# Performance work log

Measured on AMD Instinct MI355X. Metric: run time of the kernel, lower is better.

Reference implementation:

```python
import jax, jax.numpy as jnp
import numpy as np
import math

W = 256
H = 256
N = 1000
C = 1  # grayscale
ALPHA_MAX = 0.999


def _logit(p):
    return jnp.log(p) - jnp.log1p(-p)


def setup_inputs() -> dict:
    key = jax.random.key(0)
    k0, k1, k2, k3, k4 = jax.random.split(key, 5)
    means = jax.random.uniform(k0, (N, 2), dtype=jnp.float32) * W
    scales = jax.random.uniform(k1, (N, 2), dtype=jnp.float32) * 10.0 + 1.0
    quats = jax.random.uniform(k2, (N,), dtype=jnp.float32) * (2.0 * math.pi)  # rotation angle
    rgbs = _logit(jax.random.uniform(k3, (N, C), dtype=jnp.float32) * 0.3 + 0.1)
    opacities = _logit(jax.random.uniform(k4, (N,), dtype=jnp.float32) * 0.5 + 0.1)
    return {"means": means, "quats": quats, "scales": scales, "rgbs": rgbs, "opacities": opacities}


def _render(means, quats, scales, rgbs, opacities):
    # 2D covariance: Sigma = R diag(s^2) R^T, R = [[c,-s],[s,c]]
    c = jnp.cos(quats)
    s = jnp.sin(quats)
    sx2 = scales[:, 0] ** 2
    sy2 = scales[:, 1] ** 2
    a11 = c * c * sx2 + s * s * sy2
    a12 = c * s * (sx2 - sy2)
    a22 = s * s * sx2 + c * c * sy2
    det = a11 * a22 - a12 * a12
    ia = (a22 / det)[:, None, None]   # Sigma^-1 entries, broadcast over pixels
    ib = (-a12 / det)[:, None, None]
    ic = (a11 / det)[:, None, None]

    xs = jnp.arange(W, dtype=jnp.float32) + 0.5
    ys = jnp.arange(H, dtype=jnp.float32) + 0.5
    X = xs[None, :]   # [1, W] -> broadcasts to [H, W]
    Y = ys[:, None]   # [H, 1]

    dx = X[None] - means[:, 0, None, None]  # [N, H, W] (via broadcast)
    dy = Y[None] - means[:, 1, None, None]
    q = ia * dx * dx + 2.0 * ib * dx * dy + ic * dy * dy  # Mahalanobis^2, [N,H,W]

    opac = jax.nn.sigmoid(opacities)[:, None, None]
    alpha = jnp.minimum(opac * jnp.exp(-0.5 * q), ALPHA_MAX)  # [N,H,W]

    # Front-to-back compositing in index order: T_i = prod_{j<i} (1 - alpha_j)
    log_one_minus = jnp.log1p(-alpha)
    logT = jnp.cumsum(log_one_minus, axis=0) - log_one_minus  # exclusive cumsum
    weights = alpha * jnp.exp(logT)  # [N,H,W]

    colors = jax.nn.sigmoid(rgbs)  # [N,C]
    img = jnp.einsum('nhw,nc->chw', weights, colors)  # [C,H,W]
    return img[None]  # [1,C,H,W]


def reference(means, quats, scales, rgbs, opacities):
    return _render(means, quats, scales, rgbs, opacities)
```

## Files before the change

### kernel.cpp

```cpp
#include <hip/hip_runtime.h>
#include <math.h>

#define IW 256
#define IH 256
#define NG 1000
#define NSEG 4
#define SEG (NG / NSEG)
#define TILE_W 16
#define TILE_H 4
#define TILES_X (IW / TILE_W)
#define TILES_Y (IH / TILE_H)
#define ALPHA_MAX 0.999f
#define LOG2_EPS -19.93157f
#define LN2 0.6931471805599453f
#define INV_LN2 1.4426950408889634f

__global__ __launch_bounds__(256) void precompute_kernel(
    const float* __restrict__ means,
    const float* __restrict__ quats,
    const float* __restrict__ scales,
    const float* __restrict__ rgbs,
    const float* __restrict__ opacities,
    float4* __restrict__ g0,
    float4* __restrict__ g1,
    float*  __restrict__ gc)
{
    const int n = blockIdx.x * 256 + threadIdx.x;
    if (n >= NG) return;

    float2 mu = ((const float2*)means)[n];
    float2 sc = ((const float2*)scales)[n];
    float q   = quats[n];
    float opa = opacities[n];
    float rgb = rgbs[n];

    float sq, cq;
    __sincosf(q, &sq, &cq);
    float sx2 = sc.x * sc.x, sy2 = sc.y * sc.y;
    float a11 = cq * cq * sx2 + sq * sq * sy2;
    float a12 = cq * sq * (sx2 - sy2);
    float a22 = sq * sq * sx2 + cq * cq * sy2;
    float det = a11 * a22 - a12 * a12;
    float inv = INV_LN2 / det;
    float A   = -0.5f * a22 * inv;
    float B   =          a12 * inv;
    float Cc  = -0.5f * a11 * inv;
    float op  = 1.0f / (1.0f + __expf(-opa));
    float lop = __log2f(op);
    float col = 1.0f / (1.0f + __expf(-rgb));

    float t  = fmaxf((lop - LOG2_EPS) * LN2, 0.0f);
    float rx = sqrtf(2.0f * a11 * t);
    float ry = sqrtf(2.0f * a22 * t);

    g0[n] = make_float4(mu.x, mu.y, rx, ry);
    g1[n] = make_float4(A, B, Cc, lop);
    gc[n] = col;
}

__global__ __launch_bounds__(256) void splat2d_kernel(
    const float4* __restrict__ g0,
    const float4* __restrict__ g1,
    const float*  __restrict__ gc,
    float* __restrict__ out)
{
    __shared__ float4 s0[NSEG][SEG];
    __shared__ float4 s1[NSEG][SEG];
    __shared__ float2 comb[NSEG][64];

    const int tid  = threadIdx.x;
    const int lane = tid & 63;
    const int w    = tid >> 6;
    const int tx0  = blockIdx.x * TILE_W;
    const int ty0  = blockIdx.y * TILE_H;

    const float midx = (float)tx0 + 0.5f * (TILE_W - 1) + 0.5f;
    const float midy = (float)ty0 + 0.5f * (TILE_H - 1) + 0.5f;
    const float hx = 0.5f * (TILE_W - 1);
    const float hy = 0.5f * (TILE_H - 1);

    int cnt = 0;
    const int base = w * SEG;
    #pragma unroll
    for (int r = 0; r < 4; ++r) {
        const int o = r * 64 + lane;
        bool keep = false;
        float4 q0;
        if (o < SEG) {
            q0 = g0[base + o];
            keep = (fabsf(q0.x - midx) <= hx + q0.z) &&
                   (fabsf(q0.y - midy) <= hy + q0.w);
        }
        unsigned long long m = __ballot(keep);
        int rank = __popcll(m & ((1ull << lane) - 1ull));
        if (keep) {
            float4 q1 = g1[base + o];
            float col = gc[base + o];
            s0[w][cnt + rank] = make_float4(q0.x, q0.y, q1.x, q1.y);
            s1[w][cnt + rank] = make_float4(q1.z, q1.w, col, 0.0f);
        }
        cnt += __popcll(m);
    }

    const float px = (float)(tx0 + (lane & (TILE_W - 1))) + 0.5f;
    const float py = (float)(ty0 + (lane >> 4)) + 0.5f;

    float T = 1.0f;
    float accum = 0.0f;
    for (int k = 0; k < cnt; ++k) {
        float4 q0 = s0[w][k];
        float4 q1 = s1[w][k];
        float dx = px - q0.x;
        float dy = py - q0.y;
        float t  = fmaf(q0.w, dy, q0.z * dx);
        float e  = fmaf(t, dx, fmaf(q1.x * dy, dy, q1.y));
        float alpha = fminf(__builtin_amdgcn_exp2f(e), ALPHA_MAX);
        accum = fmaf(alpha * T, q1.z, accum);
        T = fmaf(-alpha, T, T);
    }
    comb[w][lane] = make_float2(accum, T);

    __syncthreads();
    if (w == 0) {
        float c = 0.0f, Tt = 1.0f;
        #pragma unroll
        for (int s = 0; s < NSEG; ++s) {
            float2 v = comb[s][lane];
            c  = fmaf(Tt, v.x, c);
            Tt *= v.y;
        }
        out[(ty0 + (lane >> 4)) * IW + tx0 + (lane & (TILE_W - 1))] = c;
    }
}

extern "C" void kernel_launch(void* const* d_in, const int* in_sizes, int n_in,
                              void* d_out, int out_size, void* d_ws, size_t ws_size,
                              hipStream_t stream) {
    const float* means     = (const float*)d_in[0];
    const float* quats     = (const float*)d_in[1];
    const float* scales    = (const float*)d_in[2];
    const float* rgbs      = (const float*)d_in[3];
    const float* opacities = (const float*)d_in[4];
    float* out = (float*)d_out;

    float4* g0 = (float4*)d_ws;
    float4* g1 = g0 + NG;
    float*  gc = (float*)(g1 + NG);

    precompute_kernel<<<dim3((NG + 255) / 256), 256, 0, stream>>>(
        means, quats, scales, rgbs, opacities, g0, g1, gc);
    splat2d_kernel<<<dim3(TILES_X, TILES_Y), 256, 0, stream>>>(
        g0, g1, gc, out);
}
```

Measured before the change: 67.89 us.

## Fuse Gaussian precompute into splat kernel with conservative scale-based pre-cull

Removes the separate precompute kernel and its workspace round trip. Each tile block now does a cheap conservative cull from the raw means and scales, using a fixed radius bound on the largest scale. It then computes covariance, opacity and colour only for the surviving candidates and applies the exact cull before staging them in shared memory. This saves a kernel launch and global traffic, but every block redoes the sincos, division and log work for its candidates, and it adds an extra shared index pass.

```diff
diff --git a/kernel.cpp b/kernel.cpp
--- a/kernel.cpp
+++ b/kernel.cpp
@@ -14,58 +14,19 @@
 #define LOG2_EPS -19.93157f
 #define LN2 0.6931471805599453f
 #define INV_LN2 1.4426950408889634f
+#define KRAD 5.2567f
 
-__global__ __launch_bounds__(256) void precompute_kernel(
+__global__ __launch_bounds__(256) void splat2d_kernel(
     const float* __restrict__ means,
     const float* __restrict__ quats,
     const float* __restrict__ scales,
     const float* __restrict__ rgbs,
     const float* __restrict__ opacities,
-    float4* __restrict__ g0,
-    float4* __restrict__ g1,
-    float*  __restrict__ gc)
-{
-    const int n = blockIdx.x * 256 + threadIdx.x;
-    if (n >= NG) return;
-
-    float2 mu = ((const float2*)means)[n];
-    float2 sc = ((const float2*)scales)[n];
-    float q   = quats[n];
-    float opa = opacities[n];
-    float rgb = rgbs[n];
-
-    float sq, cq;
-    __sincosf(q, &sq, &cq);
-    float sx2 = sc.x * sc.x, sy2 = sc.y * sc.y;
-    float a11 = cq * cq * sx2 + sq * sq * sy2;
-    float a12 = cq * sq * (sx2 - sy2);
-    float a22 = sq * sq * sx2 + cq * cq * sy2;
-    float det = a11 * a22 - a12 * a12;
-    float inv = INV_LN2 / det;
-    float A   = -0.5f * a22 * inv;
-    float B   =          a12 * inv;
-    float Cc  = -0.5f * a11 * inv;
-    float op  = 1.0f / (1.0f + __expf(-opa));
-    float lop = __log2f(op);
-    float col = 1.0f / (1.0f + __expf(-rgb));
-
-    float t  = fmaxf((lop - LOG2_EPS) * LN2, 0.0f);
-    float rx = sqrtf(2.0f * a11 * t);
-    float ry = sqrtf(2.0f * a22 * t);
-
-    g0[n] = make_float4(mu.x, mu.y, rx, ry);
-    g1[n] = make_float4(A, B, Cc, lop);
-    gc[n] = col;
-}
-
-__global__ __launch_bounds__(256) void splat2d_kernel(
-    const float4* __restrict__ g0,
-    const float4* __restrict__ g1,
-    const float*  __restrict__ gc,
     float* __restrict__ out)
 {
     __shared__ float4 s0[NSEG][SEG];
     __shared__ float4 s1[NSEG][SEG];
+    __shared__ unsigned short sidx[NSEG][SEG];
     __shared__ float2 comb[NSEG][64];
 
     const int tid  = threadIdx.x;
@@ -79,25 +40,67 @@
     const float hx = 0.5f * (TILE_W - 1);
     const float hy = 0.5f * (TILE_H - 1);
 
-    int cnt = 0;
+    const unsigned long long ltmask = (1ull << lane) - 1ull;
     const int base = w * SEG;
+
+    int m0 = 0;
     #pragma unroll
     for (int r = 0; r < 4; ++r) {
         const int o = r * 64 + lane;
+        bool k0 = false;
+        if (o < SEG) {
+            float2 mu = ((const float2*)means)[base + o];
+            float2 sc = ((const float2*)scales)[base + o];
+            float rmax = KRAD * sqrtf(sc.x * sc.x + sc.y * sc.y);
+            k0 = (fabsf(mu.x - midx) <= hx + rmax) &&
+                 (fabsf(mu.y - midy) <= hy + rmax);
+        }
+        unsigned long long m = __ballot(k0);
+        int rank = __popcll(m & ltmask);
+        if (k0) sidx[w][m0 + rank] = (unsigned short)o;
+        m0 += __popcll(m);
+    }
+
+    int cnt = 0;
+    for (int d = 0; d < m0; d += 64) {
         bool keep = false;
-        float4 q0;
-        if (o < SEG) {
-            q0 = g0[base + o];
-            keep = (fabsf(q0.x - midx) <= hx + q0.z) &&
-                   (fabsf(q0.y - midy) <= hy + q0.w);
+        float cx, cy, A, B, Cc, lop, col;
+        if (d + lane < m0) {
+            const int n = base + (int)sidx[w][d + lane];
+            float2 mu = ((const float2*)means)[n];
+            float2 sc = ((const float2*)scales)[n];
+            float q   = quats[n];
+            float opa = opacities[n];
+            float rgb = rgbs[n];
+
+            float sq, cq;
+            __sincosf(q, &sq, &cq);
+            float sx2 = sc.x * sc.x, sy2 = sc.y * sc.y;
+            float a11 = cq * cq * sx2 + sq * sq * sy2;
+            float a12 = cq * sq * (sx2 - sy2);
+            float a22 = sq * sq * sx2 + cq * cq * sy2;
+            float det = a11 * a22 - a12 * a12;
+            float inv = INV_LN2 / det;
+            A   = -0.5f * a22 * inv;
+            B   =          a12 * inv;
+            Cc  = -0.5f * a11 * inv;
+            float op = 1.0f / (1.0f + __expf(-opa));
+            lop = __log2f(op);
+            col = 1.0f / (1.0f + __expf(-rgb));
+            cx = mu.x; cy = mu.y;
+
+            float t  = fmaxf((lop - LOG2_EPS) * LN2, 0.0f);
+            float rx = sqrtf(2.0f * a11 * t);
+            float ry = sqrtf(2.0f * a22 * t);
+
+            keep = (fabsf(cx - midx) <= hx + rx) &&
+                   (fabsf(cy - midy) <= hy + ry);
         }
         unsigned long long m = __ballot(keep);
-        int rank = __popcll(m & ((1ull << lane) - 1ull));
+        int rank = __popcll(m & ltmask);
         if (keep) {
-            float4 q1 = g1[base + o];
-            float col = gc[base + o];
-            s0[w][cnt + rank] = make_float4(q0.x, q0.y, q1.x, q1.y);
-            s1[w][cnt + rank] = make_float4(q1.z, q1.w, col, 0.0f);
+            s0[w][cnt + rank] = make_float4(cx, cy, A, B);
+            s1[w][cnt + rank] = make_float4(Cc, lop, col, 0.0f);
         }
         cnt += __popcll(m);
     }
@@ -143,12 +146,6 @@
     const float* opacities = (const float*)d_in[4];
     float* out = (float*)d_out;
 
-    float4* g0 = (float4*)d_ws;
-    float4* g1 = g0 + NG;
-    float*  gc = (float*)(g1 + NG);
-
-    precompute_kernel<<<dim3((NG + 255) / 256), 256, 0, stream>>>(
-        means, quats, scales, rgbs, opacities, g0, g1, gc);
     splat2d_kernel<<<dim3(TILES_X, TILES_Y), 256, 0, stream>>>(
-        g0, g1, gc, out);
+        means, quats, scales, rgbs, opacities, out);
 }
```

Measured after the change: 66.64 us. About the same (-1.8%).
